# Performance work log

Hardware: AMD Instinct MI355X
Metric: run time of the kernel (lower is better)

The kernel has to match this reference:

```python
import jax, jax.numpy as jnp
import numpy as np

B, T, C = 32, 2048, 1024  # batch, seq_len (<= block_size), n_embd
HEAD_SIZE = 128


def setup_inputs() -> dict:
    key = jax.random.key(0)
    kx, kk, kq, kv = jax.random.split(key, 4)
    std = 0.02  # CustomLinear init: normal(0, 0.02)
    return {
        "x": jax.random.normal(kx, (B, T, C), dtype=jnp.float32),
        "Wk": jax.random.normal(kk, (HEAD_SIZE, C), dtype=jnp.float32) * std,
        "Wq": jax.random.normal(kq, (HEAD_SIZE, C), dtype=jnp.float32) * std,
        "Wv": jax.random.normal(kv, (HEAD_SIZE, C), dtype=jnp.float32) * std,
    }


def reference(x, Wk, Wq, Wv):
    # x: [B, T, C]; W*: [head_size, C] (torch Linear layout, no bias)
    Bb, Tt, Cc = x.shape
    k = jnp.einsum("btc,hc->bth", x, Wk)
    q = jnp.einsum("btc,hc->bth", x, Wq)
    v = jnp.einsum("btc,hc->bth", x, Wv)
    # NOTE: original scales by C**-0.5 (n_embd), not head_size**-0.5
    wei = jnp.einsum("bth,bsh->bts", q, k) * (Cc ** -0.5)
    causal = jnp.tril(jnp.ones((Tt, Tt), dtype=bool))  # tril[:T,:T]
    wei = jnp.where(causal, wei, -jnp.inf)
    wei = jax.nn.softmax(wei, axis=-1)
    return jnp.einsum("bts,bsh->bth", wei, v)  # [B, T, head_size]
```

## Files before the change

kernel.cpp:

```cpp
#include <hip/hip_runtime.h>
#include <hip/hip_bf16.h>

typedef __bf16 bf8_t __attribute__((ext_vector_type(8)));
typedef __bf16 bf4_t __attribute__((ext_vector_type(4)));
typedef float f4_t __attribute__((ext_vector_type(4)));

#define B_ 32
#define T_ 2048
#define C_ 1024
#define H_ 128

__global__ __launch_bounds__(256) void wconv_kernel(
    const float* __restrict__ Wk, const float* __restrict__ Wq, const float* __restrict__ Wv,
    __bf16* __restrict__ Wr)
{
    const int e  = (blockIdx.x * 256 + threadIdx.x) * 8;
    const int kk = e & 31;
    const int lr = (e >> 5) & 15;
    const int ks = (e >> 9) & 31;
    const int cg = e >> 14;
    const int col = cg * 16 + lr;
    const int k   = ks * 32 + kk;
    const float* W = (col < 128) ? Wk : (col < 256) ? Wq : Wv;
    const float* p = W + (size_t)(col & 127) * C_ + k;
    float4 f0 = *(const float4*)p;
    float4 f1 = *(const float4*)(p + 4);
    bf8_t o;
    o[0] = (__bf16)f0.x; o[1] = (__bf16)f0.y; o[2] = (__bf16)f0.z; o[3] = (__bf16)f0.w;
    o[4] = (__bf16)f1.x; o[5] = (__bf16)f1.y; o[6] = (__bf16)f1.z; o[7] = (__bf16)f1.w;
    *(bf8_t*)(Wr + e) = o;
}

__global__ __launch_bounds__(256) void proj_kernel(
    const float* __restrict__ x, const __bf16* __restrict__ Wr,
    __bf16* __restrict__ Kb, __bf16* __restrict__ Qb, __bf16* __restrict__ VtG)
{
    __shared__ __bf16 As[128 * 64];
    __shared__ __bf16 Bs[2][16 * 512];

    const int nt   = blockIdx.x % 3;
    const int m0   = (blockIdx.x / 3) * 128;
    const int tid  = threadIdx.x;
    const int lane = tid & 63;
    const int w    = tid >> 6;
    const int wqm  = w >> 1;
    const int wqn  = w & 1;
    const int lr   = lane & 15;
    const int quad = lane >> 4;

    f4_t acc[4][4];
    #pragma unroll
    for (int mi = 0; mi < 4; mi++)
        #pragma unroll
        for (int ni = 0; ni < 4; ni++) acc[mi][ni] = f4_t{0.f, 0.f, 0.f, 0.f};

    float4 pf[8];

#define LOADA(t) { _Pragma("unroll") \
    for (int i_ = 0; i_ < 8; ++i_) { \
        const int u_ = i_ * 256 + tid; \
        pf[i_] = *(const float4*)(x + (size_t)(m0 + (u_ >> 4)) * C_ + (t) * 64 + (u_ & 15) * 4); } }

#define WRITEA { _Pragma("unroll") \
    for (int i_ = 0; i_ < 8; ++i_) { \
        const int u_ = i_ * 256 + tid; \
        const int r_ = u_ >> 4; \
        float4 f_ = pf[i_]; \
        *(bf4_t*)&As[r_ * 64 + ((((u_ & 15) * 4)) ^ ((r_ & 7) * 8))] = \
            bf4_t{(__bf16)f_.x, (__bf16)f_.y, (__bf16)f_.z, (__bf16)f_.w}; } }

#define STAGEB(t, bsel) { _Pragma("unroll") \
    for (int i_ = 0; i_ < 4; ++i_) { \
        const int ci_ = i_ * 4 + w; \
        const __bf16* src_ = Wr + ((size_t)((nt * 8 + (ci_ >> 1)) * 32 + (t) * 2 + (ci_ & 1)) << 9) + lane * 8; \
        __builtin_amdgcn_global_load_lds( \
            (const __attribute__((address_space(1))) void*)src_, \
            (__attribute__((address_space(3))) void*)&Bs[bsel][ci_ << 9], 16, 0, 0); } }

    LOADA(0)
    STAGEB(0, 0)
    WRITEA
    __syncthreads();

    #pragma unroll 2
    for (int t = 0; t < 16; ++t) {
        const int bsel = t & 1;
        if (t < 15) {
            LOADA(t + 1)
            STAGEB(t + 1, bsel ^ 1)
        }
        #pragma unroll
        for (int kh = 0; kh < 2; ++kh) {
            bf8_t af[4], bfr[4];
            #pragma unroll
            for (int mi = 0; mi < 4; ++mi) {
                const int row = wqm * 64 + mi * 16 + lr;
                af[mi] = *(const bf8_t*)&As[row * 64 + ((kh * 32 + quad * 8) ^ ((row & 7) * 8))];
            }
            #pragma unroll
            for (int ni = 0; ni < 4; ++ni) {
                const int ch = (wqn * 4 + ni) * 2 + kh;
                bfr[ni] = *(const bf8_t*)&Bs[bsel][ch * 512 + lr * 32 + quad * 8];
            }
            if (nt < 2) {
                #pragma unroll
                for (int mi = 0; mi < 4; ++mi)
                    #pragma unroll
                    for (int ni = 0; ni < 4; ++ni)
                        acc[mi][ni] = __builtin_amdgcn_mfma_f32_16x16x32_bf16(af[mi], bfr[ni], acc[mi][ni], 0, 0, 0);
            } else {
                #pragma unroll
                for (int mi = 0; mi < 4; ++mi)
                    #pragma unroll
                    for (int ni = 0; ni < 4; ++ni)
                        acc[mi][ni] = __builtin_amdgcn_mfma_f32_16x16x32_bf16(bfr[ni], af[mi], acc[mi][ni], 0, 0, 0);
            }
        }
        __syncthreads();
        if (t < 15) {
            WRITEA
            __syncthreads();
        }
    }

#undef LOADA
#undef WRITEA
#undef STAGEB

    if (nt < 2) {
        __bf16* Out = nt ? Qb : Kb;
        #pragma unroll
        for (int ni = 0; ni < 4; ++ni)
            #pragma unroll
            for (int mi = 0; mi < 4; ++mi) {
                const int col = wqn * 64 + ni * 16 + lr;
                #pragma unroll
                for (int r = 0; r < 4; ++r) {
                    const int row = m0 + wqm * 64 + mi * 16 + quad * 4 + r;
                    Out[(size_t)row * H_ + col] = (__bf16)acc[mi][ni][r];
                }
            }
    } else {
        const int bb = m0 >> 11;
        const int t0 = m0 & (T_ - 1);
        #pragma unroll
        for (int ni = 0; ni < 4; ++ni)
            #pragma unroll
            for (int mi = 0; mi < 4; ++mi) {
                const int tok = t0 + wqm * 64 + mi * 16 + lr;
                #pragma unroll
                for (int r = 0; r < 4; ++r) {
                    const int h = wqn * 64 + ni * 16 + quad * 4 + r;
                    VtG[(size_t)bb * H_ * T_ + (size_t)h * T_ + tok] = (__bf16)acc[mi][ni][r];
                }
            }
    }
}

__global__ __launch_bounds__(512, 4) void flash_kernel(
    const __bf16* __restrict__ Qb, const __bf16* __restrict__ Kb,
    const __bf16* __restrict__ VtG, float* __restrict__ Out)
{
    __shared__ __bf16 Ks[64][136];
    __shared__ __bf16 Vt[128][72];
    __shared__ __bf16 Ps[128][72];

    const int qt = (blockIdx.y < 16) ? (15 - blockIdx.x) : blockIdx.x;
    const int b  = blockIdx.y;
    const size_t kqbase = (size_t)b * T_ * H_;
    const size_t vbase  = (size_t)b * H_ * T_;

    const int tid  = threadIdx.x;
    const int lane = tid & 63;
    const int w    = tid >> 6;
    const int lr   = lane & 15;
    const int quad = lane >> 4;

    bf8_t qf[4];
    {
        const __bf16* qp = Qb + kqbase + (size_t)(qt * 128 + w * 16 + lr) * H_ + quad * 8;
        #pragma unroll
        for (int ks = 0; ks < 4; ks++) qf[ks] = *(const bf8_t*)(qp + ks * 32);
    }

    f4_t o[8];
    #pragma unroll
    for (int n = 0; n < 8; n++) o[n] = f4_t{0.f, 0.f, 0.f, 0.f};
    float ls[4] = {0.f, 0.f, 0.f, 0.f};

    const float sc = 0.03125f * 1.4426950408889634f;
    const int jmax = 2 * qt + 1;

    const int kRow0 = tid >> 4,          kC0 = (tid & 15) << 3;
    const int kRow1 = (tid + 512) >> 4,  kC1 = ((tid + 512) & 15) << 3;
    const int vH0 = tid >> 3,            vS0 = (tid & 7) << 3;
    const int vH1 = (tid + 512) >> 3,    vS1 = ((tid + 512) & 7) << 3;

    bf8_t kr0 = *(const bf8_t*)(Kb + kqbase + (size_t)kRow0 * H_ + kC0);
    bf8_t kr1 = *(const bf8_t*)(Kb + kqbase + (size_t)kRow1 * H_ + kC1);
    bf8_t vr0 = *(const bf8_t*)(VtG + vbase + (size_t)vH0 * T_ + vS0);
    bf8_t vr1 = *(const bf8_t*)(VtG + vbase + (size_t)vH1 * T_ + vS1);

    for (int j = 0; j <= jmax; j++) {
        __syncthreads();
        *(bf8_t*)&Ks[kRow0][kC0] = kr0;
        *(bf8_t*)&Ks[kRow1][kC1] = kr1;
        *(bf8_t*)&Vt[vH0][vS0]   = vr0;
        *(bf8_t*)&Vt[vH1][vS1]   = vr1;
        __syncthreads();
        if (j < jmax) {
            const int s0 = (j + 1) * 64;
            kr0 = *(const bf8_t*)(Kb + kqbase + (size_t)(s0 + kRow0) * H_ + kC0);
            kr1 = *(const bf8_t*)(Kb + kqbase + (size_t)(s0 + kRow1) * H_ + kC1);
            vr0 = *(const bf8_t*)(VtG + vbase + (size_t)vH0 * T_ + s0 + vS0);
            vr1 = *(const bf8_t*)(VtG + vbase + (size_t)vH1 * T_ + s0 + vS1);
        }
        if (j == jmax && w < 4) continue;

        f4_t s4[4];
        #pragma unroll
        for (int n = 0; n < 4; n++) s4[n] = f4_t{0.f, 0.f, 0.f, 0.f};
        #pragma unroll
        for (int ks = 0; ks < 4; ks++)
            for (int n = 0; n < 4; n++) {
                bf8_t kf = *(const bf8_t*)&Ks[n * 16 + lr][ks * 32 + quad * 8];
                s4[n] = __builtin_amdgcn_mfma_f32_16x16x32_bf16(qf[ks], kf, s4[n], 0, 0, 0);
            }

        const bool domask = (j - 2 * qt) == (w >> 2);
        const int rowg = qt * 128 + w * 16 + quad * 4;
        #pragma unroll
        for (int n = 0; n < 4; n++) {
            const int colg = j * 64 + n * 16 + lr;
            #pragma unroll
            for (int r = 0; r < 4; r++) {
                float p = __builtin_exp2f(s4[n][r] * sc);
                if (domask && colg > rowg + r) p = 0.f;
                ls[r] += p;
                Ps[w * 16 + quad * 4 + r][n * 16 + lr] = (__bf16)p;
            }
        }

        #pragma unroll
        for (int ks = 0; ks < 2; ks++) {
            bf8_t pf2 = *(const bf8_t*)&Ps[w * 16 + lr][ks * 32 + quad * 8];
            #pragma unroll
            for (int n = 0; n < 8; n++) {
                bf8_t vf = *(const bf8_t*)&Vt[n * 16 + lr][ks * 32 + quad * 8];
                o[n] = __builtin_amdgcn_mfma_f32_16x16x32_bf16(pf2, vf, o[n], 0, 0, 0);
            }
        }
    }

    float inv[4];
    #pragma unroll
    for (int r = 0; r < 4; r++) {
        float v = ls[r];
        v += __shfl_xor(v, 1);
        v += __shfl_xor(v, 2);
        v += __shfl_xor(v, 4);
        v += __shfl_xor(v, 8);
        inv[r] = 1.f / v;
    }
    #pragma unroll
    for (int n = 0; n < 8; n++) {
        const int col = n * 16 + lr;
        #pragma unroll
        for (int r = 0; r < 4; r++) {
            const int row = qt * 128 + w * 16 + quad * 4 + r;
            Out[kqbase + (size_t)row * H_ + col] = o[n][r] * inv[r];
        }
    }
}

extern "C" void kernel_launch(void* const* d_in, const int* in_sizes, int n_in,
                              void* d_out, int out_size, void* d_ws, size_t ws_size,
                              hipStream_t stream) {
    const float* x  = (const float*)d_in[0];
    const float* Wk = (const float*)d_in[1];
    const float* Wq = (const float*)d_in[2];
    const float* Wv = (const float*)d_in[3];
    float* out = (float*)d_out;

    const size_t n_kqv = (size_t)B_ * T_ * H_;
    __bf16* Kb  = (__bf16*)d_ws;
    __bf16* Qb  = Kb + n_kqv;
    __bf16* VtG = Qb + n_kqv;
    __bf16* Wr  = VtG + n_kqv;

    wconv_kernel<<<dim3(192), 256, 0, stream>>>(Wk, Wq, Wv, Wr);
    proj_kernel<<<dim3(512 * 3), 256, 0, stream>>>(x, Wr, Kb, Qb, VtG);
    flash_kernel<<<dim3(16, B_), 512, 0, stream>>>(Qb, Kb, VtG, out);
}
```

Before: 478.4 us.

## Give each flash wave two query row tiles and remap projection blocks across XCDs

```diff
diff --git a/kernel.cpp b/kernel.cpp
--- a/kernel.cpp
+++ b/kernel.cpp
@@ -38,8 +38,11 @@
     __shared__ __bf16 As[128 * 64];
     __shared__ __bf16 Bs[2][16 * 512];
 
-    const int nt   = blockIdx.x % 3;
-    const int m0   = (blockIdx.x / 3) * 128;
+    const int bid  = blockIdx.x;
+    const int xcd  = bid & 7;
+    const int slot = bid >> 3;
+    const int nt   = slot % 3;
+    const int m0   = ((slot / 3) * 8 + xcd) * 128;
     const int tid  = threadIdx.x;
     const int lane = tid & 63;
     const int w    = tid >> 6;
@@ -157,7 +160,7 @@
     }
 }
 
-__global__ __launch_bounds__(512, 4) void flash_kernel(
+__global__ __launch_bounds__(256, 2) void flash_kernel(
     const __bf16* __restrict__ Qb, const __bf16* __restrict__ Kb,
     const __bf16* __restrict__ VtG, float* __restrict__ Out)
 {
@@ -176,101 +179,125 @@
     const int lr   = lane & 15;
     const int quad = lane >> 4;
 
-    bf8_t qf[4];
-    {
-        const __bf16* qp = Qb + kqbase + (size_t)(qt * 128 + w * 16 + lr) * H_ + quad * 8;
-        #pragma unroll
-        for (int ks = 0; ks < 4; ks++) qf[ks] = *(const bf8_t*)(qp + ks * 32);
-    }
-
-    f4_t o[8];
-    #pragma unroll
-    for (int n = 0; n < 8; n++) o[n] = f4_t{0.f, 0.f, 0.f, 0.f};
-    float ls[4] = {0.f, 0.f, 0.f, 0.f};
+    bf8_t qf[2][4];
+    #pragma unroll
+    for (int m = 0; m < 2; m++) {
+        const __bf16* qp = Qb + kqbase + (size_t)(qt * 128 + w * 32 + m * 16 + lr) * H_ + quad * 8;
+        #pragma unroll
+        for (int ks = 0; ks < 4; ks++) qf[m][ks] = *(const bf8_t*)(qp + ks * 32);
+    }
+
+    f4_t o[2][8];
+    #pragma unroll
+    for (int m = 0; m < 2; m++)
+        #pragma unroll
+        for (int n = 0; n < 8; n++) o[m][n] = f4_t{0.f, 0.f, 0.f, 0.f};
+    float ls[2] = {0.f, 0.f};
 
     const float sc = 0.03125f * 1.4426950408889634f;
     const int jmax = 2 * qt + 1;
 
-    const int kRow0 = tid >> 4,          kC0 = (tid & 15) << 3;
-    const int kRow1 = (tid + 512) >> 4,  kC1 = ((tid + 512) & 15) << 3;
-    const int vH0 = tid >> 3,            vS0 = (tid & 7) << 3;
-    const int vH1 = (tid + 512) >> 3,    vS1 = ((tid + 512) & 7) << 3;
-
-    bf8_t kr0 = *(const bf8_t*)(Kb + kqbase + (size_t)kRow0 * H_ + kC0);
-    bf8_t kr1 = *(const bf8_t*)(Kb + kqbase + (size_t)kRow1 * H_ + kC1);
-    bf8_t vr0 = *(const bf8_t*)(VtG + vbase + (size_t)vH0 * T_ + vS0);
-    bf8_t vr1 = *(const bf8_t*)(VtG + vbase + (size_t)vH1 * T_ + vS1);
+    int kR[4], kC[4], vH[4], vS[4];
+    #pragma unroll
+    for (int i = 0; i < 4; i++) {
+        const int u = tid + i * 256;
+        kR[i] = u >> 4;  kC[i] = (u & 15) << 3;
+        vH[i] = u >> 3;  vS[i] = (u & 7) << 3;
+    }
+    bf8_t kr[4], vr[4];
+    #pragma unroll
+    for (int i = 0; i < 4; i++) {
+        kr[i] = *(const bf8_t*)(Kb + kqbase + (size_t)kR[i] * H_ + kC[i]);
+        vr[i] = *(const bf8_t*)(VtG + vbase + (size_t)vH[i] * T_ + vS[i]);
+    }
 
     for (int j = 0; j <= jmax; j++) {
         __syncthreads();
-        *(bf8_t*)&Ks[kRow0][kC0] = kr0;
-        *(bf8_t*)&Ks[kRow1][kC1] = kr1;
-        *(bf8_t*)&Vt[vH0][vS0]   = vr0;
-        *(bf8_t*)&Vt[vH1][vS1]   = vr1;
+        #pragma unroll
+        for (int i = 0; i < 4; i++) {
+            *(bf8_t*)&Ks[kR[i]][kC[i]] = kr[i];
+            *(bf8_t*)&Vt[vH[i]][vS[i]] = vr[i];
+        }
         __syncthreads();
         if (j < jmax) {
             const int s0 = (j + 1) * 64;
-            kr0 = *(const bf8_t*)(Kb + kqbase + (size_t)(s0 + kRow0) * H_ + kC0);
-            kr1 = *(const bf8_t*)(Kb + kqbase + (size_t)(s0 + kRow1) * H_ + kC1);
-            vr0 = *(const bf8_t*)(VtG + vbase + (size_t)vH0 * T_ + s0 + vS0);
-            vr1 = *(const bf8_t*)(VtG + vbase + (size_t)vH1 * T_ + s0 + vS1);
-        }
-        if (j == jmax && w < 4) continue;
-
-        f4_t s4[4];
-        #pragma unroll
-        for (int n = 0; n < 4; n++) s4[n] = f4_t{0.f, 0.f, 0.f, 0.f};
+            #pragma unroll
+            for (int i = 0; i < 4; i++) {
+                kr[i] = *(const bf8_t*)(Kb + kqbase + (size_t)(s0 + kR[i]) * H_ + kC[i]);
+                vr[i] = *(const bf8_t*)(VtG + vbase + (size_t)vH[i] * T_ + s0 + vS[i]);
+            }
+        }
+        if (j == jmax && w < 2) continue;
+
+        f4_t s4[2][4];
+        #pragma unroll
+        for (int m = 0; m < 2; m++)
+            #pragma unroll
+            for (int n = 0; n < 4; n++) s4[m][n] = f4_t{0.f, 0.f, 0.f, 0.f};
         #pragma unroll
         for (int ks = 0; ks < 4; ks++)
+            #pragma unroll
             for (int n = 0; n < 4; n++) {
                 bf8_t kf = *(const bf8_t*)&Ks[n * 16 + lr][ks * 32 + quad * 8];
-                s4[n] = __builtin_amdgcn_mfma_f32_16x16x32_bf16(qf[ks], kf, s4[n], 0, 0, 0);
-            }
-
-        const bool domask = (j - 2 * qt) == (w >> 2);
-        const int rowg = qt * 128 + w * 16 + quad * 4;
-        #pragma unroll
-        for (int n = 0; n < 4; n++) {
-            const int colg = j * 64 + n * 16 + lr;
-            #pragma unroll
-            for (int r = 0; r < 4; r++) {
-                float p = __builtin_exp2f(s4[n][r] * sc);
-                if (domask && colg > rowg + r) p = 0.f;
-                ls[r] += p;
-                Ps[w * 16 + quad * 4 + r][n * 16 + lr] = (__bf16)p;
+                s4[0][n] = __builtin_amdgcn_mfma_f32_16x16x32_bf16(kf, qf[0][ks], s4[0][n], 0, 0, 0);
+                s4[1][n] = __builtin_amdgcn_mfma_f32_16x16x32_bf16(kf, qf[1][ks], s4[1][n], 0, 0, 0);
+            }
+
+        const bool domask = (j == 2 * qt + (w >> 1));
+        const int jrel = (j - 2 * qt) * 64;
+        #pragma unroll
+        for (int m = 0; m < 2; m++) {
+            const int qg = w * 32 + m * 16 + lr;
+            #pragma unroll
+            for (int n = 0; n < 4; n++) {
+                bf4_t pk;
+                #pragma unroll
+                for (int r = 0; r < 4; r++) {
+                    float p = __builtin_exp2f(s4[m][n][r] * sc);
+                    const int kg = jrel + n * 16 + quad * 4 + r;
+                    if (domask && kg > qg) p = 0.f;
+                    ls[m] += p;
+                    pk[r] = (__bf16)p;
+                }
+                *(bf4_t*)&Ps[w * 32 + m * 16 + lr][n * 16 + quad * 4] = pk;
             }
         }
 
         #pragma unroll
         for (int ks = 0; ks < 2; ks++) {
-            bf8_t pf2 = *(const bf8_t*)&Ps[w * 16 + lr][ks * 32 + quad * 8];
+            bf8_t pf0 = *(const bf8_t*)&Ps[w * 32 + lr][ks * 32 + quad * 8];
+            bf8_t pf1 = *(const bf8_t*)&Ps[w * 32 + 16 + lr][ks * 32 + quad * 8];
             #pragma unroll
             for (int n = 0; n < 8; n++) {
                 bf8_t vf = *(const bf8_t*)&Vt[n * 16 + lr][ks * 32 + quad * 8];
-                o[n] = __builtin_amdgcn_mfma_f32_16x16x32_bf16(pf2, vf, o[n], 0, 0, 0);
-            }
-        }
-    }
-
-    float inv[4];
-    #pragma unroll
-    for (int r = 0; r < 4; r++) {
-        float v = ls[r];
-        v += __shfl_xor(v, 1);
-        v += __shfl_xor(v, 2);
-        v += __shfl_xor(v, 4);
-        v += __shfl_xor(v, 8);
-        inv[r] = 1.f / v;
-    }
-    #pragma unroll
-    for (int n = 0; n < 8; n++) {
-        const int col = n * 16 + lr;
-        #pragma unroll
-        for (int r = 0; r < 4; r++) {
-            const int row = qt * 128 + w * 16 + quad * 4 + r;
-            Out[kqbase + (size_t)row * H_ + col] = o[n][r] * inv[r];
-        }
-    }
+                o[0][n] = __builtin_amdgcn_mfma_f32_16x16x32_bf16(pf0, vf, o[0][n], 0, 0, 0);
+                o[1][n] = __builtin_amdgcn_mfma_f32_16x16x32_bf16(pf1, vf, o[1][n], 0, 0, 0);
+            }
+        }
+    }
+
+    float inv[2][4];
+    #pragma unroll
+    for (int m = 0; m < 2; m++) {
+        float v = ls[m];
+        v += __shfl_xor(v, 16);
+        v += __shfl_xor(v, 32);
+        const float iv = 1.f / v;
+        #pragma unroll
+        for (int r = 0; r < 4; r++)
+            inv[m][r] = __shfl(iv, quad * 4 + r);
+    }
+    #pragma unroll
+    for (int m = 0; m < 2; m++)
+        #pragma unroll
+        for (int n = 0; n < 8; n++) {
+            const int col = n * 16 + lr;
+            #pragma unroll
+            for (int r = 0; r < 4; r++) {
+                const int row = qt * 128 + w * 32 + m * 16 + quad * 4 + r;
+                Out[kqbase + (size_t)row * H_ + col] = o[m][n][r] * inv[m][r];
+            }
+        }
 }
 
 extern "C" void kernel_launch(void* const* d_in, const int* in_sizes, int n_in,
@@ -290,5 +317,5 @@
 
     wconv_kernel<<<dim3(192), 256, 0, stream>>>(Wk, Wq, Wv, Wr);
     proj_kernel<<<dim3(512 * 3), 256, 0, stream>>>(x, Wr, Kb, Qb, VtG);
-    flash_kernel<<<dim3(16, B_), 512, 0, stream>>>(Qb, Kb, VtG, out);
+    flash_kernel<<<dim3(16, B_), 256, 0, stream>>>(Qb, Kb, VtG, out);
 }
```

New measurement: 472.9 us. Within noise of the previous version (-1.1%).
